# Kernel optimization log

Measured on AMD Instinct MI355X. Metric: run time of the kernel, lower is better.

The kernel has to match this reference:

```python
import jax, jax.numpy as jnp
import numpy as np

N_ATOMS = 768
BOX_L = 30.0
CUTOFF = 5.0


def _cp(a, b, c):
    # numpy equivalent of torch.cartesian_prod for 1-D inputs
    g = np.meshgrid(a, b, c, indexing='ij')
    return np.stack(g, axis=-1).reshape(-1, 3)


def get_shifts_np(box, pbc, cutoff):
    # host-side mirror of TorchNeighborList._get_shifts (data-dependent shapes)
    recip = np.linalg.inv(box).T
    inv_len = np.linalg.norm(recip, axis=1)
    nrep = np.where(pbc, np.ceil(cutoff * inv_len).astype(np.int64), 0)
    r1 = np.arange(1, nrep[0] + 1)
    r2 = np.arange(1, nrep[1] + 1)
    r3 = np.arange(1, nrep[2] + 1)
    o = np.zeros(1, dtype=np.int64)
    blocks = [_cp(r1, r2, r3), _cp(r1, r2, o), _cp(r1, r2, -r3),
              _cp(r1, o, r3), _cp(r1, o, o), _cp(r1, o, -r3),
              _cp(r1, -r2, r3), _cp(r1, -r2, o), _cp(r1, -r2, -r3),
              _cp(o, r2, r3), _cp(o, r2, o), _cp(o, r2, -r3), _cp(o, o, r3)]
    return np.concatenate(blocks, axis=0).astype(np.int32)


def setup_inputs() -> dict:
    key = jax.random.key(0)
    positions = jax.random.uniform(key, (N_ATOMS, 3), dtype=jnp.float32) * BOX_L
    box = jnp.eye(3, dtype=jnp.float32) * BOX_L
    shifts = jnp.asarray(get_shifts_np(np.eye(3) * BOX_L, np.array([True, True, True]), CUTOFF))  # (13, 3)
    return {"positions": positions, "box": box, "shifts": shifts, "cutoff": CUTOFF}


def reference(positions, box, shifts, cutoff):
    N = positions.shape[0]
    S = shifts.shape[0]
    # central-cell unique pairs i<j (torch.combinations)
    iu, ju = jnp.triu_indices(N, k=1)
    # shifted candidates: cartesian_prod(shift_index, i, j)
    shift_idx = jnp.repeat(jnp.arange(S), N * N)
    pi_s = jnp.tile(jnp.repeat(jnp.arange(N), N), S)
    pj_s = jnp.tile(jnp.arange(N), S * N)
    pi_all = jnp.concatenate([iu, pi_s])          # (P,)
    pj_all = jnp.concatenate([ju, pj_s])          # (P,)
    shifts_all = jnp.concatenate([jnp.zeros((iu.shape[0], 3), dtype=shifts.dtype), shifts[shift_idx]])  # (P,3)
    shift_vals = shifts_all.astype(box.dtype) @ box
    Rij = positions[pi_all] - positions[pj_all] + shift_vals  # (P,3)
    d = jnp.linalg.norm(Rij, axis=1)
    mask = d < cutoff
    # bidirectional pairs (torch.cat of (i,j) and (j,i)), offsets negated for the first half
    bi_i = jnp.concatenate([pi_all, pj_all])
    bi_j = jnp.concatenate([pj_all, pi_all])
    bi_off = jnp.concatenate([-shifts_all, shifts_all])
    bi_mask = jnp.concatenate([mask, mask])
    # jit-compatible compaction: sort by idx_i with invalid entries pushed to the end
    sort_key = jnp.where(bi_mask, bi_i, N)
    order = jnp.argsort(sort_key)  # jax sort is stable
    valid = bi_mask[order]
    idx_i = jnp.where(valid, bi_i[order], -1)
    idx_j = jnp.where(valid, bi_j[order], -1)
    offset = (bi_off[order].astype(box.dtype) @ box) * valid[:, None].astype(box.dtype)
    return idx_i, idx_j, offset, valid
```

## Files before the change

### kernel.cpp

```cpp
#include <hip/hip_runtime.h>

#pragma clang fp contract(off)


#define MAX_SHIFTS 64
#define FILL_ITERS 16

typedef float f32x4 __attribute__((ext_vector_type(4)));

__device__ __forceinline__ bool pv_fwd(float fx, float fy, float fz,
                                       const float* __restrict__ pos, int j,
                                       float sx, float sy, float sz, float cutoff) {
  float dx = fx - pos[j * 3 + 0] + sx;
  float dy = fy - pos[j * 3 + 1] + sy;
  float dz = fz - pos[j * 3 + 2] + sz;
  float d2 = dx * dx + dy * dy + dz * dz;
  return sqrtf(d2) < cutoff;
}

__device__ __forceinline__ bool pv_bwd(const float* __restrict__ pos, int a,
                                       float fx, float fy, float fz,
                                       float sx, float sy, float sz, float cutoff) {
  float dx = pos[a * 3 + 0] - fx + sx;
  float dy = pos[a * 3 + 1] - fy + sy;
  float dz = pos[a * 3 + 2] - fz + sz;
  float d2 = dx * dx + dy * dy + dz * dz;
  return sqrtf(d2) < cutoff;
}

__device__ __forceinline__ bool axis_ok(float lo, float hi, float cutpad) {
  return (hi > -cutpad) && (lo < cutpad);
}

__global__ __launch_bounds__(256) void k_phase1(
    const float* __restrict__ pos, const float* __restrict__ box,
    const int* __restrict__ shifts, const float* __restrict__ cutp,
    int N, int S, int* __restrict__ count,
    float* __restrict__ out, long M, long n4, int NFB) {
  int t = threadIdx.x;

  if ((int)blockIdx.x < NFB) {
    long k_lo = (long)blockIdx.x * (256L * FILL_ITERS);
    long k_hi = k_lo + 256L * FILL_ITERS;
    if (k_hi > n4) k_hi = n4;
    long m4 = (2 * M) >> 2;
    const f32x4 neg = {-1.f, -1.f, -1.f, -1.f};
    const f32x4 zer = {0.f, 0.f, 0.f, 0.f};
    f32x4* __restrict__ out4 = (f32x4*)out;

    if (k_hi - k_lo == 256L * FILL_ITERS && (k_hi <= m4 || k_lo >= m4)) {
      f32x4 val = (k_lo < m4) ? neg : zer;
      f32x4* __restrict__ p = out4 + k_lo + t;
#pragma unroll
      for (int it = 0; it < FILL_ITERS; it++) p[(long)it * 256] = val;
    } else {
      for (long k = k_lo + t; k < k_hi; k += 256)
        out4[k] = (k < m4) ? neg : zer;
    }
    return;
  }

  __shared__ float sv[MAX_SHIFTS * 3];
  __shared__ float bred[4][6];
  __shared__ int rf[4], rb[4];
  int atom = (int)blockIdx.x - NFB;
  int w = t >> 6;
  float cut = cutp[0];
  float cutpad = cut + fmaxf(cut * 1e-5f, 1e-5f);

  for (int s = t; s < S; s += 256) {
    float s0 = (float)shifts[s * 3 + 0];
    float s1 = (float)shifts[s * 3 + 1];
    float s2 = (float)shifts[s * 3 + 2];
    sv[s * 3 + 0] = s0 * box[0] + s1 * box[3] + s2 * box[6];
    sv[s * 3 + 1] = s0 * box[1] + s1 * box[4] + s2 * box[7];
    sv[s * 3 + 2] = s0 * box[2] + s1 * box[5] + s2 * box[8];
  }

  float mnx = 1e30f, mny = 1e30f, mnz = 1e30f, mxx = -1e30f, mxy = -1e30f, mxz = -1e30f;
  for (int i = t; i < N; i += 256) {
    float x = pos[3 * i + 0], y = pos[3 * i + 1], z = pos[3 * i + 2];
    mnx = fminf(mnx, x); mny = fminf(mny, y); mnz = fminf(mnz, z);
    mxx = fmaxf(mxx, x); mxy = fmaxf(mxy, y); mxz = fmaxf(mxz, z);
  }
  for (int off = 32; off; off >>= 1) {
    mnx = fminf(mnx, __shfl_xor(mnx, off)); mny = fminf(mny, __shfl_xor(mny, off));
    mnz = fminf(mnz, __shfl_xor(mnz, off)); mxx = fmaxf(mxx, __shfl_xor(mxx, off));
    mxy = fmaxf(mxy, __shfl_xor(mxy, off)); mxz = fmaxf(mxz, __shfl_xor(mxz, off));
  }
  if ((t & 63) == 0) {
    bred[w][0] = mnx; bred[w][1] = mny; bred[w][2] = mnz;
    bred[w][3] = mxx; bred[w][4] = mxy; bred[w][5] = mxz;
  }
  __syncthreads();
  mnx = bred[0][0]; mny = bred[0][1]; mnz = bred[0][2];
  mxx = bred[0][3]; mxy = bred[0][4]; mxz = bred[0][5];
  for (int ww = 1; ww < 4; ww++) {
    mnx = fminf(mnx, bred[ww][0]); mny = fminf(mny, bred[ww][1]); mnz = fminf(mnz, bred[ww][2]);
    mxx = fmaxf(mxx, bred[ww][3]); mxy = fmaxf(mxy, bred[ww][4]); mxz = fmaxf(mxz, bred[ww][5]);
  }

  float pix = pos[3 * atom + 0], piy = pos[3 * atom + 1], piz = pos[3 * atom + 2];
  int cf = 0, cb = 0;
  for (int j = atom + 1 + t; j < N; j += 256)
    if (pv_fwd(pix, piy, piz, pos, j, 0.f, 0.f, 0.f, cut)) cf++;
  for (int a = t; a < atom; a += 256)
    if (pv_bwd(pos, a, pix, piy, piz, 0.f, 0.f, 0.f, cut)) cb++;

  for (int s = 0; s < S; s++) {
    float svx = sv[3 * s + 0], svy = sv[3 * s + 1], svz = sv[3 * s + 2];
    bool af = axis_ok((pix - mxx) + svx, (pix - mnx) + svx, cutpad) &&
              axis_ok((piy - mxy) + svy, (piy - mny) + svy, cutpad) &&
              axis_ok((piz - mxz) + svz, (piz - mnz) + svz, cutpad);
    if (af) {
      for (int j = t; j < N; j += 256)
        if (pv_fwd(pix, piy, piz, pos, j, svx, svy, svz, cut)) cf++;
    }
    bool ab = axis_ok((mnx - pix) + svx, (mxx - pix) + svx, cutpad) &&
              axis_ok((mny - piy) + svy, (mxy - piy) + svy, cutpad) &&
              axis_ok((mnz - piz) + svz, (mxz - piz) + svz, cutpad);
    if (ab) {
      for (int a = t; a < N; a += 256)
        if (pv_bwd(pos, a, pix, piy, piz, svx, svy, svz, cut)) cb++;
    }
  }
  for (int off = 32; off; off >>= 1) {
    cf += __shfl_down(cf, off);
    cb += __shfl_down(cb, off);
  }
  if ((t & 63) == 0) { rf[w] = cf; rb[w] = cb; }
  __syncthreads();
  if (t == 0) {
    count[2 * atom + 0] = rf[0] + rf[1] + rf[2] + rf[3];
    count[2 * atom + 1] = rb[0] + rb[1] + rb[2] + rb[3];
  }
}

__global__ __launch_bounds__(256) void k_rows(
    const float* __restrict__ pos, const float* __restrict__ box,
    const int* __restrict__ shifts, const float* __restrict__ cutp,
    int N, int S, const int* __restrict__ count,
    float* __restrict__ out, long M) {
  __shared__ float sv[MAX_SHIFTS * 3];
  int t = threadIdx.x;
  int lane = t & 63, w = t >> 6;
  int n2 = 2 * N;
  float cut = cutp[0];
  float cutpad = cut + fmaxf(cut * 1e-5f, 1e-5f);

  for (int s = t; s < S; s += 256) {
    float s0 = (float)shifts[s * 3 + 0];
    float s1 = (float)shifts[s * 3 + 1];
    float s2 = (float)shifts[s * 3 + 2];
    sv[s * 3 + 0] = s0 * box[0] + s1 * box[3] + s2 * box[6];
    sv[s * 3 + 1] = s0 * box[1] + s1 * box[4] + s2 * box[7];
    sv[s * 3 + 2] = s0 * box[2] + s1 * box[5] + s2 * box[8];
  }
  __syncthreads();

  int g = blockIdx.x * 4 + w;
  if (g >= n2) return;
  int atom = g >> 1;
  int dir = g & 1;

  float mnx = 1e30f, mny = 1e30f, mnz = 1e30f, mxx = -1e30f, mxy = -1e30f, mxz = -1e30f;
  for (int i = lane; i < N; i += 64) {
    float x = pos[3 * i + 0], y = pos[3 * i + 1], z = pos[3 * i + 2];
    mnx = fminf(mnx, x); mny = fminf(mny, y); mnz = fminf(mnz, z);
    mxx = fmaxf(mxx, x); mxy = fmaxf(mxy, y); mxz = fmaxf(mxz, z);
  }
  for (int off = 32; off; off >>= 1) {
    mnx = fminf(mnx, __shfl_xor(mnx, off)); mny = fminf(mny, __shfl_xor(mny, off));
    mnz = fminf(mnz, __shfl_xor(mnz, off)); mxx = fmaxf(mxx, __shfl_xor(mxx, off));
    mxy = fmaxf(mxy, __shfl_xor(mxy, off)); mxz = fmaxf(mxz, __shfl_xor(mxz, off));
  }

  int pre = 0;
  for (int i = lane; i < g; i += 64) pre += count[i];
  for (int off = 32; off; off >>= 1) pre += __shfl_xor(pre, off);
  long base = pre;

  float* __restrict__ out_i = out;
  float* __restrict__ out_j = out + M;
  float* __restrict__ out_off = out + 2 * M;
  float* __restrict__ out_v = out + 5 * M;

  float pix = pos[3 * atom + 0], piy = pos[3 * atom + 1], piz = pos[3 * atom + 2];
  float fatom = (float)atom;
  int running = 0;

  {
    int n = (dir == 0) ? (N - 1 - atom) : atom;
    int j0 = (dir == 0) ? (atom + 1) : 0;
    float oz0 = (dir == 0) ? -0.0f : 0.0f;
    for (int c0 = 0; c0 < n; c0 += 64) {
      int c = c0 + lane;
      bool v = false;
      int other = j0 + c;
      if (c < n) {
        v = (dir == 0) ? pv_fwd(pix, piy, piz, pos, other, 0.f, 0.f, 0.f, cut)
                       : pv_bwd(pos, other, pix, piy, piz, 0.f, 0.f, 0.f, cut);
      }
      unsigned long long m = __ballot(v);
      if (v) {
        int rank = __popcll(m & ((1ULL << lane) - 1ULL));
        long row = base + running + rank;
        out_i[row] = fatom;
        out_j[row] = (float)other;
        out_off[row * 3 + 0] = oz0;
        out_off[row * 3 + 1] = oz0;
        out_off[row * 3 + 2] = oz0;
        out_v[row] = 1.0f;
      }
      running += __popcll(m);
    }
  }
  for (int s = 0; s < S; s++) {
    float svx = sv[3 * s + 0], svy = sv[3 * s + 1], svz = sv[3 * s + 2];
    bool active;
    if (dir == 0) {
      active = axis_ok((pix - mxx) + svx, (pix - mnx) + svx, cutpad) &&
               axis_ok((piy - mxy) + svy, (piy - mny) + svy, cutpad) &&
               axis_ok((piz - mxz) + svz, (piz - mnz) + svz, cutpad);
    } else {
      active = axis_ok((mnx - pix) + svx, (mxx - pix) + svx, cutpad) &&
               axis_ok((mny - piy) + svy, (mxy - piy) + svy, cutpad) &&
               axis_ok((mnz - piz) + svz, (mxz - piz) + svz, cutpad);
    }
    if (!active) continue;
    float ox = (dir == 0) ? -svx : svx;
    float oy = (dir == 0) ? -svy : svy;
    float oz = (dir == 0) ? -svz : svz;
    for (int c0 = 0; c0 < N; c0 += 64) {
      int other = c0 + lane;
      bool v = false;
      if (other < N) {
        v = (dir == 0) ? pv_fwd(pix, piy, piz, pos, other, svx, svy, svz, cut)
                       : pv_bwd(pos, other, pix, piy, piz, svx, svy, svz, cut);
      }
      unsigned long long m = __ballot(v);
      if (v) {
        int rank = __popcll(m & ((1ULL << lane) - 1ULL));
        long row = base + running + rank;
        out_i[row] = fatom;
        out_j[row] = (float)other;
        out_off[row * 3 + 0] = ox;
        out_off[row * 3 + 1] = oy;
        out_off[row * 3 + 2] = oz;
        out_v[row] = 1.0f;
      }
      running += __popcll(m);
    }
  }
}

extern "C" void kernel_launch(void* const* d_in, const int* in_sizes, int n_in,
                              void* d_out, int out_size, void* d_ws, size_t ws_size,
                              hipStream_t stream) {
  const float* pos = (const float*)d_in[0];
  const float* box = (const float*)d_in[1];
  const int* shifts = (const int*)d_in[2];
  const float* cutp = (const float*)d_in[3];
  int N = in_sizes[0] / 3;
  int S = in_sizes[2] / 3;
  long M = (long)out_size / 6;
  float* out = (float*)d_out;

  int* count = (int*)d_ws;

  long n4 = (long)out_size / 4;
  int NFB = (int)((n4 + (256L * FILL_ITERS) - 1) / (256L * FILL_ITERS));
  int NWB = (2 * N + 3) / 4;

  hipLaunchKernelGGL(k_phase1, dim3(NFB + N), dim3(256), 0, stream,
                     pos, box, shifts, cutp, N, S, count, out, M, n4, NFB);
  hipLaunchKernelGGL(k_rows, dim3(NWB), dim3(256), 0, stream,
                     pos, box, shifts, cutp, N, S, count, out, M);
}
```

Before: 112.0 us.

## Move padding fill into row-writing kernel and skip writing rows that get valid data

The fill of the output with padding values (-1 for indices, 0 for offsets and valid) moves from the counting kernel into the second kernel, running in extra grid-stride blocks alongside the row writers. Each fill block first sums the per-atom counts to get the total number of valid rows. It then writes padding only past that total in each output segment, so rows the writers will overwrite are no longer written twice. This removes redundant global stores but adds a count reduction per fill block and a fixed grid of 4096 fill blocks.

```diff
diff --git a/kernel.cpp b/kernel.cpp
--- a/kernel.cpp
+++ b/kernel.cpp
@@ -4,9 +4,10 @@
 
 
 #define MAX_SHIFTS 64
-#define FILL_ITERS 16
+#define NFB 4096
 
 typedef float f32x4 __attribute__((ext_vector_type(4)));
+typedef int i32x4 __attribute__((ext_vector_type(4)));
 
 __device__ __forceinline__ bool pv_fwd(float fx, float fy, float fz,
                                        const float* __restrict__ pos, int j,
@@ -32,38 +33,15 @@
   return (hi > -cutpad) && (lo < cutpad);
 }
 
-__global__ __launch_bounds__(256) void k_phase1(
+__global__ __launch_bounds__(256) void k_count(
     const float* __restrict__ pos, const float* __restrict__ box,
     const int* __restrict__ shifts, const float* __restrict__ cutp,
-    int N, int S, int* __restrict__ count,
-    float* __restrict__ out, long M, long n4, int NFB) {
-  int t = threadIdx.x;
-
-  if ((int)blockIdx.x < NFB) {
-    long k_lo = (long)blockIdx.x * (256L * FILL_ITERS);
-    long k_hi = k_lo + 256L * FILL_ITERS;
-    if (k_hi > n4) k_hi = n4;
-    long m4 = (2 * M) >> 2;
-    const f32x4 neg = {-1.f, -1.f, -1.f, -1.f};
-    const f32x4 zer = {0.f, 0.f, 0.f, 0.f};
-    f32x4* __restrict__ out4 = (f32x4*)out;
-
-    if (k_hi - k_lo == 256L * FILL_ITERS && (k_hi <= m4 || k_lo >= m4)) {
-      f32x4 val = (k_lo < m4) ? neg : zer;
-      f32x4* __restrict__ p = out4 + k_lo + t;
-#pragma unroll
-      for (int it = 0; it < FILL_ITERS; it++) p[(long)it * 256] = val;
-    } else {
-      for (long k = k_lo + t; k < k_hi; k += 256)
-        out4[k] = (k < m4) ? neg : zer;
-    }
-    return;
-  }
-
+    int N, int S, int* __restrict__ count) {
   __shared__ float sv[MAX_SHIFTS * 3];
   __shared__ float bred[4][6];
   __shared__ int rf[4], rb[4];
-  int atom = (int)blockIdx.x - NFB;
+  int atom = blockIdx.x;
+  int t = threadIdx.x;
   int w = t >> 6;
   float cut = cutp[0];
   float cutpad = cut + fmaxf(cut * 1e-5f, 1e-5f);
@@ -136,120 +114,157 @@
   }
 }
 
-__global__ __launch_bounds__(256) void k_rows(
+__global__ __launch_bounds__(256) void k_main(
     const float* __restrict__ pos, const float* __restrict__ box,
     const int* __restrict__ shifts, const float* __restrict__ cutp,
     int N, int S, const int* __restrict__ count,
-    float* __restrict__ out, long M) {
+    float* __restrict__ out, long M, long n4, int NWB) {
   __shared__ float sv[MAX_SHIFTS * 3];
   int t = threadIdx.x;
   int lane = t & 63, w = t >> 6;
   int n2 = 2 * N;
-  float cut = cutp[0];
-  float cutpad = cut + fmaxf(cut * 1e-5f, 1e-5f);
-
-  for (int s = t; s < S; s += 256) {
-    float s0 = (float)shifts[s * 3 + 0];
-    float s1 = (float)shifts[s * 3 + 1];
-    float s2 = (float)shifts[s * 3 + 2];
-    sv[s * 3 + 0] = s0 * box[0] + s1 * box[3] + s2 * box[6];
-    sv[s * 3 + 1] = s0 * box[1] + s1 * box[4] + s2 * box[7];
-    sv[s * 3 + 2] = s0 * box[2] + s1 * box[5] + s2 * box[8];
-  }
-  __syncthreads();
-
-  int g = blockIdx.x * 4 + w;
-  if (g >= n2) return;
-  int atom = g >> 1;
-  int dir = g & 1;
-
-  float mnx = 1e30f, mny = 1e30f, mnz = 1e30f, mxx = -1e30f, mxy = -1e30f, mxz = -1e30f;
-  for (int i = lane; i < N; i += 64) {
-    float x = pos[3 * i + 0], y = pos[3 * i + 1], z = pos[3 * i + 2];
-    mnx = fminf(mnx, x); mny = fminf(mny, y); mnz = fminf(mnz, z);
-    mxx = fmaxf(mxx, x); mxy = fmaxf(mxy, y); mxz = fmaxf(mxz, z);
-  }
-  for (int off = 32; off; off >>= 1) {
-    mnx = fminf(mnx, __shfl_xor(mnx, off)); mny = fminf(mny, __shfl_xor(mny, off));
-    mnz = fminf(mnz, __shfl_xor(mnz, off)); mxx = fmaxf(mxx, __shfl_xor(mxx, off));
-    mxy = fmaxf(mxy, __shfl_xor(mxy, off)); mxz = fmaxf(mxz, __shfl_xor(mxz, off));
-  }
-
-  int pre = 0;
-  for (int i = lane; i < g; i += 64) pre += count[i];
-  for (int off = 32; off; off >>= 1) pre += __shfl_xor(pre, off);
-  long base = pre;
-
-  float* __restrict__ out_i = out;
-  float* __restrict__ out_j = out + M;
-  float* __restrict__ out_off = out + 2 * M;
-  float* __restrict__ out_v = out + 5 * M;
-
-  float pix = pos[3 * atom + 0], piy = pos[3 * atom + 1], piz = pos[3 * atom + 2];
-  float fatom = (float)atom;
-  int running = 0;
-
-  {
-    int n = (dir == 0) ? (N - 1 - atom) : atom;
-    int j0 = (dir == 0) ? (atom + 1) : 0;
-    float oz0 = (dir == 0) ? -0.0f : 0.0f;
-    for (int c0 = 0; c0 < n; c0 += 64) {
-      int c = c0 + lane;
-      bool v = false;
-      int other = j0 + c;
-      if (c < n) {
-        v = (dir == 0) ? pv_fwd(pix, piy, piz, pos, other, 0.f, 0.f, 0.f, cut)
-                       : pv_bwd(pos, other, pix, piy, piz, 0.f, 0.f, 0.f, cut);
-      }
-      unsigned long long m = __ballot(v);
-      if (v) {
-        int rank = __popcll(m & ((1ULL << lane) - 1ULL));
-        long row = base + running + rank;
-        out_i[row] = fatom;
-        out_j[row] = (float)other;
-        out_off[row * 3 + 0] = oz0;
-        out_off[row * 3 + 1] = oz0;
-        out_off[row * 3 + 2] = oz0;
-        out_v[row] = 1.0f;
-      }
-      running += __popcll(m);
-    }
-  }
-  for (int s = 0; s < S; s++) {
-    float svx = sv[3 * s + 0], svy = sv[3 * s + 1], svz = sv[3 * s + 2];
-    bool active;
-    if (dir == 0) {
-      active = axis_ok((pix - mxx) + svx, (pix - mnx) + svx, cutpad) &&
-               axis_ok((piy - mxy) + svy, (piy - mny) + svy, cutpad) &&
-               axis_ok((piz - mxz) + svz, (piz - mnz) + svz, cutpad);
-    } else {
-      active = axis_ok((mnx - pix) + svx, (mxx - pix) + svx, cutpad) &&
-               axis_ok((mny - piy) + svy, (mxy - piy) + svy, cutpad) &&
-               axis_ok((mnz - piz) + svz, (mxz - piz) + svz, cutpad);
-    }
-    if (!active) continue;
-    float ox = (dir == 0) ? -svx : svx;
-    float oy = (dir == 0) ? -svy : svy;
-    float oz = (dir == 0) ? -svz : svz;
-    for (int c0 = 0; c0 < N; c0 += 64) {
-      int other = c0 + lane;
-      bool v = false;
-      if (other < N) {
-        v = (dir == 0) ? pv_fwd(pix, piy, piz, pos, other, svx, svy, svz, cut)
-                       : pv_bwd(pos, other, pix, piy, piz, svx, svy, svz, cut);
-      }
-      unsigned long long m = __ballot(v);
-      if (v) {
-        int rank = __popcll(m & ((1ULL << lane) - 1ULL));
-        long row = base + running + rank;
-        out_i[row] = fatom;
-        out_j[row] = (float)other;
-        out_off[row * 3 + 0] = ox;
-        out_off[row * 3 + 1] = oy;
-        out_off[row * 3 + 2] = oz;
-        out_v[row] = 1.0f;
-      }
-      running += __popcll(m);
+
+  if ((int)blockIdx.x < NWB) {
+    float cut = cutp[0];
+    float cutpad = cut + fmaxf(cut * 1e-5f, 1e-5f);
+    for (int s = t; s < S; s += 256) {
+      float s0 = (float)shifts[s * 3 + 0];
+      float s1 = (float)shifts[s * 3 + 1];
+      float s2 = (float)shifts[s * 3 + 2];
+      sv[s * 3 + 0] = s0 * box[0] + s1 * box[3] + s2 * box[6];
+      sv[s * 3 + 1] = s0 * box[1] + s1 * box[4] + s2 * box[7];
+      sv[s * 3 + 2] = s0 * box[2] + s1 * box[5] + s2 * box[8];
+    }
+    __syncthreads();
+    int g = blockIdx.x * 4 + w;
+    if (g >= n2) return;
+    int atom = g >> 1;
+    int dir = g & 1;
+
+    float mnx = 1e30f, mny = 1e30f, mnz = 1e30f, mxx = -1e30f, mxy = -1e30f, mxz = -1e30f;
+    for (int i = lane; i < N; i += 64) {
+      float x = pos[3 * i + 0], y = pos[3 * i + 1], z = pos[3 * i + 2];
+      mnx = fminf(mnx, x); mny = fminf(mny, y); mnz = fminf(mnz, z);
+      mxx = fmaxf(mxx, x); mxy = fmaxf(mxy, y); mxz = fmaxf(mxz, z);
+    }
+    for (int off = 32; off; off >>= 1) {
+      mnx = fminf(mnx, __shfl_xor(mnx, off)); mny = fminf(mny, __shfl_xor(mny, off));
+      mnz = fminf(mnz, __shfl_xor(mnz, off)); mxx = fmaxf(mxx, __shfl_xor(mxx, off));
+      mxy = fmaxf(mxy, __shfl_xor(mxy, off)); mxz = fmaxf(mxz, __shfl_xor(mxz, off));
+    }
+
+    int pre = 0;
+    for (int i = lane; i < g; i += 64) pre += count[i];
+    for (int off = 32; off; off >>= 1) pre += __shfl_xor(pre, off);
+    long base = pre;
+
+    float* __restrict__ out_i = out;
+    float* __restrict__ out_j = out + M;
+    float* __restrict__ out_off = out + 2 * M;
+    float* __restrict__ out_v = out + 5 * M;
+
+    float pix = pos[3 * atom + 0], piy = pos[3 * atom + 1], piz = pos[3 * atom + 2];
+    float fatom = (float)atom;
+    float cut2 = cut;
+    int running = 0;
+
+    {
+      int n = (dir == 0) ? (N - 1 - atom) : atom;
+      int j0 = (dir == 0) ? (atom + 1) : 0;
+      float oz0 = (dir == 0) ? -0.0f : 0.0f;
+      for (int c0 = 0; c0 < n; c0 += 64) {
+        int c = c0 + lane;
+        bool v = false;
+        int other = j0 + c;
+        if (c < n) {
+          v = (dir == 0) ? pv_fwd(pix, piy, piz, pos, other, 0.f, 0.f, 0.f, cut2)
+                         : pv_bwd(pos, other, pix, piy, piz, 0.f, 0.f, 0.f, cut2);
+        }
+        unsigned long long m = __ballot(v);
+        if (v) {
+          int rank = __popcll(m & ((1ULL << lane) - 1ULL));
+          long row = base + running + rank;
+          out_i[row] = fatom;
+          out_j[row] = (float)other;
+          out_off[row * 3 + 0] = oz0;
+          out_off[row * 3 + 1] = oz0;
+          out_off[row * 3 + 2] = oz0;
+          out_v[row] = 1.0f;
+        }
+        running += __popcll(m);
+      }
+    }
+    for (int s = 0; s < S; s++) {
+      float svx = sv[3 * s + 0], svy = sv[3 * s + 1], svz = sv[3 * s + 2];
+      bool active;
+      if (dir == 0) {
+        active = axis_ok((pix - mxx) + svx, (pix - mnx) + svx, cutpad) &&
+                 axis_ok((piy - mxy) + svy, (piy - mny) + svy, cutpad) &&
+                 axis_ok((piz - mxz) + svz, (piz - mnz) + svz, cutpad);
+      } else {
+        active = axis_ok((mnx - pix) + svx, (mxx - pix) + svx, cutpad) &&
+                 axis_ok((mny - piy) + svy, (mxy - piy) + svy, cutpad) &&
+                 axis_ok((mnz - piz) + svz, (mxz - piz) + svz, cutpad);
+      }
+      if (!active) continue;
+      float ox = (dir == 0) ? -svx : svx;
+      float oy = (dir == 0) ? -svy : svy;
+      float oz = (dir == 0) ? -svz : svz;
+      for (int c0 = 0; c0 < N; c0 += 64) {
+        int other = c0 + lane;
+        bool v = false;
+        if (other < N) {
+          v = (dir == 0) ? pv_fwd(pix, piy, piz, pos, other, svx, svy, svz, cut2)
+                         : pv_bwd(pos, other, pix, piy, piz, svx, svy, svz, cut2);
+        }
+        unsigned long long m = __ballot(v);
+        if (v) {
+          int rank = __popcll(m & ((1ULL << lane) - 1ULL));
+          long row = base + running + rank;
+          out_i[row] = fatom;
+          out_j[row] = (float)other;
+          out_off[row * 3 + 0] = ox;
+          out_off[row * 3 + 1] = oy;
+          out_off[row * 3 + 2] = oz;
+          out_v[row] = 1.0f;
+        }
+        running += __popcll(m);
+      }
+    }
+  } else {
+    int tot = 0;
+    const i32x4* __restrict__ c4 = (const i32x4*)count;
+    int nq = n2 >> 2;
+    for (int i = lane; i < nq; i += 64) {
+      i32x4 v = c4[i];
+      tot += v.x + v.y + v.z + v.w;
+    }
+    for (int off = 32; off; off >>= 1) tot += __shfl_xor(tot, off);
+    long total = tot;
+
+    long E0 = total;
+    long E1 = M + total;
+    long E2 = 2 * M + 3 * total;
+    long E3 = 5 * M + total;
+    long m2 = 2 * M, m5 = 5 * M;
+    const f32x4 neg = {-1.f, -1.f, -1.f, -1.f};
+    const f32x4 zer = {0.f, 0.f, 0.f, 0.f};
+    f32x4* __restrict__ out4 = (f32x4*)out;
+
+    long fidx = ((long)blockIdx.x - NWB) * 256 + t;
+    long fstride = (long)NFB * 256;
+    for (long k = fidx; k < n4; k += fstride) {
+      long e = k << 2;
+      long ve = (e < M) ? E0 : ((e < m2) ? E1 : ((e < m5) ? E2 : E3));
+      if (e + 4 <= ve) continue;
+      bool isneg = (e < m2);
+      if (e >= ve) {
+        out4[k] = isneg ? neg : zer;
+      } else {
+        float dv = isneg ? -1.f : 0.f;
+        for (int q = 0; q < 4; q++)
+          if (e + q >= ve) out[e + q] = dv;
+      }
     }
   }
 }
@@ -269,11 +284,10 @@
   int* count = (int*)d_ws;
 
   long n4 = (long)out_size / 4;
-  int NFB = (int)((n4 + (256L * FILL_ITERS) - 1) / (256L * FILL_ITERS));
   int NWB = (2 * N + 3) / 4;
 
-  hipLaunchKernelGGL(k_phase1, dim3(NFB + N), dim3(256), 0, stream,
-                     pos, box, shifts, cutp, N, S, count, out, M, n4, NFB);
-  hipLaunchKernelGGL(k_rows, dim3(NWB), dim3(256), 0, stream,
-                     pos, box, shifts, cutp, N, S, count, out, M);
-}
+  hipLaunchKernelGGL(k_count, dim3(N), dim3(256), 0, stream,
+                     pos, box, shifts, cutp, N, S, count);
+  hipLaunchKernelGGL(k_main, dim3(NWB + NFB), dim3(256), 0, stream,
+                     pos, box, shifts, cutp, N, S, count, out, M, n4, NWB);
+}
```

After: 110.3 us. About the same (-1.6%).
